# Performance work log

Measured on AMD Instinct MI355X. Metric: run time of the kernel, lower is better.

The kernel has to match this reference:

```python
import jax, jax.numpy as jnp
import numpy as np

COMMITMENT_COST = 0.25


def setup_inputs() -> dict:
    key = jax.random.key(0)
    k1, k2 = jax.random.split(key)
    B, L, D, K = 32, 1024, 128, 1024
    z = jax.random.normal(k1, (B, L, D), dtype=jnp.float32)
    # torch init: uniform_(-1/num_embeddings, 1/num_embeddings)
    codebook = jax.random.uniform(k2, (K, D), dtype=jnp.float32,
                                  minval=-1.0 / K, maxval=1.0 / K)
    return {"z": z, "codebook": codebook}


def reference(z, codebook):
    D = codebook.shape[1]
    flat_z = z.reshape(-1, D)                         # [N, D]
    # squared-euclidean distances, expanded form (same math as torch)
    distances = (jnp.sum(flat_z ** 2, axis=1, keepdims=True)
                 + jnp.sum(codebook ** 2, axis=1)
                 - 2.0 * flat_z @ codebook.T)         # [N, K]
    encoding_indices = jnp.argmin(distances, axis=1)  # [N]
    quantized = codebook[encoding_indices].reshape(z.shape)
    # straight-through estimator
    z_q = z + jax.lax.stop_gradient(quantized - z)
    q_loss = jnp.mean((jax.lax.stop_gradient(quantized) - z) ** 2)
    e_loss = jnp.mean((quantized - jax.lax.stop_gradient(z)) ** 2)
    vq_loss = q_loss + COMMITMENT_COST * e_loss
    return z_q, vq_loss, encoding_indices
```

## Files before the change

kernel.cpp:

```cpp
#include <hip/hip_runtime.h>
#include <float.h>

#define NTOK 32768
#define DDIM 128
#define KCODES 1024
#define TT 128
#define NTHR 512
#define NCHUNK 16
#define CHUNK_BYTES 32768

typedef __attribute__((ext_vector_type(8))) short short8v;
typedef __attribute__((ext_vector_type(4))) float f32x4;

__device__ __forceinline__ float nofuse(float x) { asm volatile("" : "+v"(x)); return x; }

__device__ __forceinline__ unsigned short bf16rne(float x) {
    unsigned int u = __float_as_uint(x);
    unsigned int r = u + 0x7FFFu + ((u >> 16) & 1u);
    return (unsigned short)(r >> 16);
}
__device__ __forceinline__ float bf16tof(unsigned short h) {
    return __uint_as_float(((unsigned int)h) << 16);
}

__device__ __forceinline__ void cvt8(const float* f, uint4& hw, uint4& lw) {
    unsigned int h[8], l[8];
    #pragma unroll
    for (int e = 0; e < 8; ++e) {
        unsigned short hh = bf16rne(f[e]);
        unsigned short ll = bf16rne(f[e] - bf16tof(hh));
        h[e] = hh; l[e] = ll;
    }
    hw = make_uint4(h[0] | (h[1] << 16), h[2] | (h[3] << 16),
                    h[4] | (h[5] << 16), h[6] | (h[7] << 16));
    lw = make_uint4(l[0] | (l[1] << 16), l[2] | (l[3] << 16),
                    l[4] | (l[5] << 16), l[6] | (l[7] << 16));
}

__device__ __forceinline__ short8v as_s8(uint4 v) { return __builtin_bit_cast(short8v, v); }

__global__ __launch_bounds__(256)
void pack_cb(const float* __restrict__ cb, float* __restrict__ cnorm,
             char* __restrict__ cbS) {
    const int tid = threadIdx.x;
    const int row = blockIdx.x * 256 + tid;
    const float* p = cb + (size_t)row * DDIM;
    {
        float r[8];
        {
            float4 a = *(const float4*)p, c = *(const float4*)(p + 4);
            float v[8] = {a.x, a.y, a.z, a.w, c.x, c.y, c.z, c.w};
            #pragma unroll
            for (int j = 0; j < 8; ++j) r[j] = nofuse(v[j] * v[j]);
        }
        #pragma unroll
        for (int i = 8; i < DDIM; i += 8) {
            float4 a = *(const float4*)(p + i), c = *(const float4*)(p + i + 4);
            float v[8] = {a.x, a.y, a.z, a.w, c.x, c.y, c.z, c.w};
            #pragma unroll
            for (int j = 0; j < 8; ++j) r[j] = nofuse(r[j] + nofuse(v[j] * v[j]));
        }
        float s01 = nofuse(r[0] + r[1]), s23 = nofuse(r[2] + r[3]);
        float s45 = nofuse(r[4] + r[5]), s67 = nofuse(r[6] + r[7]);
        cnorm[row] = nofuse(nofuse(s01 + s23) + nofuse(s45 + s67));
    }
    char* base = cbS + (size_t)(row >> 6) * CHUNK_BYTES + (size_t)(row & 63) * 256;
    const int swz = (row & 7) << 4;
    #pragma unroll
    for (int d8 = 0; d8 < 16; ++d8) {
        float4 a = *(const float4*)(p + d8 * 8), c = *(const float4*)(p + d8 * 8 + 4);
        float f[8] = {a.x, a.y, a.z, a.w, c.x, c.y, c.z, c.w};
        uint4 hw, lw;
        cvt8(f, hw, lw);
        int col = (d8 << 4) ^ swz;
        *(uint4*)(base + col) = hw;
        *(uint4*)(base + 16384 + col) = lw;
    }
}

__global__ __launch_bounds__(NTHR, 2)
void dist_argmin(const float* __restrict__ z, const float* __restrict__ cb,
                 const float* __restrict__ cnorm, const char* __restrict__ cbS,
                 float* __restrict__ zq, float* __restrict__ idxf_out,
                 float* __restrict__ partials) {
    __shared__ __align__(16) char buf[2 * CHUNK_BYTES];
    __shared__ float zn_s[TT];
    __shared__ float cn_s[KCODES];
    __shared__ float red_v[TT * 2];
    __shared__ int   red_i[TT * 2];
    __shared__ int   bidx[TT];
    __shared__ float smf[8];

    const int tid  = threadIdx.x;
    const int lane = tid & 63;
    const int wave = tid >> 6;
    const int wy   = wave & 3;
    const int wx   = wave >> 2;
    const int l15  = lane & 15;
    const int l4   = lane >> 4;
    const int t0   = blockIdx.x * TT;

    auto stage = [&](int slot, int chunk) {
        const char* g = cbS + (size_t)chunk * CHUNK_BYTES + wave * 4096 + (lane << 4);
        char* ldst = buf + slot * CHUNK_BYTES + wave * 4096;
        #pragma unroll
        for (int j = 0; j < 4; ++j)
            __builtin_amdgcn_global_load_lds(
                (const __attribute__((address_space(1))) unsigned int*)(g + j * 1024),
                (__attribute__((address_space(3))) unsigned int*)(ldst + j * 1024),
                16, 0, 0);
    };

    short8v Ah[2][4], Al[2][4];
    #pragma unroll
    for (int tf = 0; tf < 2; ++tf) {
        int row = t0 + wy * 32 + tf * 16 + l15;
        const float* p = z + (size_t)row * DDIM;
        #pragma unroll
        for (int ks = 0; ks < 4; ++ks) {
            float4 a = *(const float4*)(p + ks * 32 + l4 * 8);
            float4 c = *(const float4*)(p + ks * 32 + l4 * 8 + 4);
            float f[8] = {a.x, a.y, a.z, a.w, c.x, c.y, c.z, c.w};
            uint4 hw, lw;
            cvt8(f, hw, lw);
            Ah[tf][ks] = as_s8(hw);
            Al[tf][ks] = as_s8(lw);
        }
    }

    stage(0, 0);

    cn_s[tid]       = cnorm[tid];
    cn_s[tid + 512] = cnorm[tid + 512];

    if (tid < TT) {
        const float* p = z + (size_t)(t0 + tid) * DDIM;
        float r[8];
        {
            float4 a = *(const float4*)p, c = *(const float4*)(p + 4);
            float v[8] = {a.x, a.y, a.z, a.w, c.x, c.y, c.z, c.w};
            #pragma unroll
            for (int j = 0; j < 8; ++j) r[j] = nofuse(v[j] * v[j]);
        }
        #pragma unroll
        for (int i = 8; i < DDIM; i += 8) {
            float4 a = *(const float4*)(p + i), c = *(const float4*)(p + i + 4);
            float v[8] = {a.x, a.y, a.z, a.w, c.x, c.y, c.z, c.w};
            #pragma unroll
            for (int j = 0; j < 8; ++j) r[j] = nofuse(r[j] + nofuse(v[j] * v[j]));
        }
        float s01 = nofuse(r[0] + r[1]), s23 = nofuse(r[2] + r[3]);
        float s45 = nofuse(r[4] + r[5]), s67 = nofuse(r[6] + r[7]);
        zn_s[tid] = nofuse(nofuse(s01 + s23) + nofuse(s45 + s67));
    }
    __syncthreads();

    float znr[8];
    #pragma unroll
    for (int tf = 0; tf < 2; ++tf)
        #pragma unroll
        for (int rg = 0; rg < 4; ++rg)
            znr[tf * 4 + rg] = zn_s[wy * 32 + tf * 16 + l4 * 4 + rg];

    float minv[8]; int mini[8];
    #pragma unroll
    for (int i = 0; i < 8; ++i) { minv[i] = FLT_MAX; mini[i] = 0; }

    auto compute = [&](int slot, int it) {
        const char* bb = buf + slot * CHUNK_BYTES;
        short8v Bh[2][4], Bl[2][4];
        #pragma unroll
        for (int cf = 0; cf < 2; ++cf) {
            int r = wx * 32 + cf * 16 + l15;
            int swz = (r & 7) << 4;
            #pragma unroll
            for (int ks = 0; ks < 4; ++ks) {
                int off = r * 256 + ((((ks * 4 + l4) << 4)) ^ swz);
                Bh[cf][ks] = *(const short8v*)(bb + off);
                Bl[cf][ks] = *(const short8v*)(bb + 16384 + off);
            }
        }
        asm volatile("s_waitcnt lgkmcnt(0)" ::: "memory");
        __builtin_amdgcn_sched_barrier(0);

        f32x4 acc[2][2];
        #pragma unroll
        for (int tf = 0; tf < 2; ++tf)
            #pragma unroll
            for (int cf = 0; cf < 2; ++cf)
                acc[tf][cf] = (f32x4){0.f, 0.f, 0.f, 0.f};
        #pragma unroll
        for (int ks = 0; ks < 4; ++ks)
            #pragma unroll
            for (int tf = 0; tf < 2; ++tf)
                #pragma unroll
                for (int cf = 0; cf < 2; ++cf) {
                    acc[tf][cf] = __builtin_amdgcn_mfma_f32_16x16x32_bf16(Ah[tf][ks], Bh[cf][ks], acc[tf][cf], 0, 0, 0);
                    acc[tf][cf] = __builtin_amdgcn_mfma_f32_16x16x32_bf16(Ah[tf][ks], Bl[cf][ks], acc[tf][cf], 0, 0, 0);
                    acc[tf][cf] = __builtin_amdgcn_mfma_f32_16x16x32_bf16(Al[tf][ks], Bh[cf][ks], acc[tf][cf], 0, 0, 0);
                }
        #pragma unroll
        for (int cf = 0; cf < 2; ++cf) {
            int kk = it * 64 + wx * 32 + cf * 16 + l15;
            float cn = cn_s[kk];
            #pragma unroll
            for (int tf = 0; tf < 2; ++tf)
                #pragma unroll
                for (int rg = 0; rg < 4; ++rg) {
                    float s = nofuse(znr[tf * 4 + rg] + cn);
                    float dist = fmaf(-2.0f, acc[tf][cf][rg], s);
                    int ii = tf * 4 + rg;
                    if (dist < minv[ii]) { minv[ii] = dist; mini[ii] = kk; }
                }
        }
    };

    int cur = 0;
    #pragma unroll 1
    for (int t = 0; t < NCHUNK - 1; ++t) {
        stage(cur ^ 1, t + 1);
        asm volatile("s_waitcnt vmcnt(4)" ::: "memory");
        __builtin_amdgcn_s_barrier();
        compute(cur, t);
        asm volatile("s_waitcnt lgkmcnt(0)" ::: "memory");
        __builtin_amdgcn_s_barrier();
        cur ^= 1;
    }
    asm volatile("s_waitcnt vmcnt(0)" ::: "memory");
    __builtin_amdgcn_s_barrier();
    compute(cur, NCHUNK - 1);

    #pragma unroll
    for (int i = 0; i < 8; ++i) {
        float bv = minv[i]; int bi = mini[i];
        #pragma unroll
        for (int off = 1; off < 16; off <<= 1) {
            float ov = __shfl_xor(bv, off);
            int   oi = __shfl_xor(bi, off);
            if (ov < bv || (ov == bv && oi < bi)) { bv = ov; bi = oi; }
        }
        if (l15 == 0) {
            int tok = wy * 32 + (i >> 2) * 16 + l4 * 4 + (i & 3);
            red_v[tok * 2 + wx] = bv;
            red_i[tok * 2 + wx] = bi;
        }
    }
    __syncthreads();
    if (tid < TT) {
        float bv = red_v[tid * 2]; int bi = red_i[tid * 2];
        float v1 = red_v[tid * 2 + 1]; int i1 = red_i[tid * 2 + 1];
        if (v1 < bv || (v1 == bv && i1 < bi)) { bv = v1; bi = i1; }
        bidx[tid] = bi;
        idxf_out[t0 + tid] = (float)bi;
    }
    __syncthreads();

    float s = 0.0f;
    #pragma unroll
    for (int ft = 0; ft < 8; ++ft) {
        int g = ft * NTHR + tid;
        int t = g >> 5;
        int d4 = g & 31;
        int k = bidx[t];
        float4 q4 = *(const float4*)(cb + (size_t)k * DDIM + 4 * d4);
        float4 z4 = *(const float4*)(z + (size_t)(t0 + t) * DDIM + 4 * d4);
        *(float4*)(zq + (size_t)(t0 + t) * DDIM + 4 * d4) = q4;
        float dx = q4.x - z4.x, dy = q4.y - z4.y, dz = q4.z - z4.z, dw = q4.w - z4.w;
        s += dx * dx + dy * dy + dz * dz + dw * dw;
    }
    #pragma unroll
    for (int off = 32; off > 0; off >>= 1) s += __shfl_down(s, off);
    if ((tid & 63) == 0) smf[tid >> 6] = s;
    __syncthreads();
    if (tid == 0) {
        float tot = 0.0f;
        #pragma unroll
        for (int w = 0; w < 8; ++w) tot += smf[w];
        partials[blockIdx.x] = tot;
    }
}

__global__ void loss_final(const float* __restrict__ partials, float* __restrict__ out_loss) {
    double s = 0.0;
    for (int i = threadIdx.x; i < NTOK / TT; i += 256) s += (double)partials[i];
    #pragma unroll
    for (int off = 32; off > 0; off >>= 1) s += __shfl_down(s, off);
    __shared__ double sm[4];
    int lane = threadIdx.x & 63, wv = threadIdx.x >> 6;
    if (lane == 0) sm[wv] = s;
    __syncthreads();
    if (threadIdx.x == 0) {
        double tot = sm[0] + sm[1] + sm[2] + sm[3];
        out_loss[0] = (float)(tot * 1.25 / (double)((size_t)NTOK * DDIM));
    }
}

extern "C" void kernel_launch(void* const* d_in, const int* in_sizes, int n_in,
                              void* d_out, int out_size, void* d_ws, size_t ws_size,
                              hipStream_t stream) {
    const float* z  = (const float*)d_in[0];
    const float* cb = (const float*)d_in[1];
    float* out = (float*)d_out;
    float* zq   = out;
    float* loss = out + (size_t)NTOK * DDIM;
    float* idxf = loss + 1;

    float* cnorm    = (float*)d_ws;
    float* partials = cnorm + KCODES;
    char*  cbS      = (char*)(partials + 256);

    pack_cb<<<KCODES / 256, 256, 0, stream>>>(cb, cnorm, cbS);
    dist_argmin<<<NTOK / TT, NTHR, 0, stream>>>(z, cb, cnorm, cbS, zq, idxf, partials);
    loss_final<<<1, 256, 0, stream>>>(partials, loss);
}
```

Baseline: 123.8 us.

## Remap waves to 2x4 grid with 64 tokens per wave, shrink pack_cb blocks

The wave tiling of the distance GEMM changes from a 4x2 grid (32 tokens x 32 codes per wave) to a 2x4 grid (64 tokens x 16 codes per wave). The z fragments are held in more registers and each B fragment is loaded per k-step and reused across four token tiles, which cuts LDS reads of the codebook per wave. The cross-wave argmin reduction widens to four partials per token, and token norms are read from LDS inside the epilogue instead of being cached in registers. Separately, pack_cb is launched with 64-thread blocks to spread its 1024 rows over more CUs. The larger A register footprint risks spills or lower occupancy under the (512,2) launch bounds.

```diff
diff --git a/kernel.cpp b/kernel.cpp
--- a/kernel.cpp
+++ b/kernel.cpp
@@ -39,11 +39,10 @@
 
 __device__ __forceinline__ short8v as_s8(uint4 v) { return __builtin_bit_cast(short8v, v); }
 
-__global__ __launch_bounds__(256)
+__global__ __launch_bounds__(64)
 void pack_cb(const float* __restrict__ cb, float* __restrict__ cnorm,
              char* __restrict__ cbS) {
-    const int tid = threadIdx.x;
-    const int row = blockIdx.x * 256 + tid;
+    const int row = blockIdx.x * 64 + threadIdx.x;
     const float* p = cb + (size_t)row * DDIM;
     {
         float r[8];
@@ -86,16 +85,16 @@
     __shared__ __align__(16) char buf[2 * CHUNK_BYTES];
     __shared__ float zn_s[TT];
     __shared__ float cn_s[KCODES];
-    __shared__ float red_v[TT * 2];
-    __shared__ int   red_i[TT * 2];
+    __shared__ float red_v[TT * 4];
+    __shared__ int   red_i[TT * 4];
     __shared__ int   bidx[TT];
     __shared__ float smf[8];
 
     const int tid  = threadIdx.x;
     const int lane = tid & 63;
     const int wave = tid >> 6;
-    const int wy   = wave & 3;
-    const int wx   = wave >> 2;
+    const int wy   = wave >> 2;
+    const int wx   = wave & 3;
     const int l15  = lane & 15;
     const int l4   = lane >> 4;
     const int t0   = blockIdx.x * TT;
@@ -111,10 +110,10 @@
                 16, 0, 0);
     };
 
-    short8v Ah[2][4], Al[2][4];
-    #pragma unroll
-    for (int tf = 0; tf < 2; ++tf) {
-        int row = t0 + wy * 32 + tf * 16 + l15;
+    short8v Ah[4][4], Al[4][4];
+    #pragma unroll
+    for (int tf = 0; tf < 4; ++tf) {
+        int row = t0 + wy * 64 + tf * 16 + l15;
         const float* p = z + (size_t)row * DDIM;
         #pragma unroll
         for (int ks = 0; ks < 4; ++ks) {
@@ -155,64 +154,45 @@
     }
     __syncthreads();
 
-    float znr[8];
-    #pragma unroll
-    for (int tf = 0; tf < 2; ++tf)
-        #pragma unroll
-        for (int rg = 0; rg < 4; ++rg)
-            znr[tf * 4 + rg] = zn_s[wy * 32 + tf * 16 + l4 * 4 + rg];
-
-    float minv[8]; int mini[8];
-    #pragma unroll
-    for (int i = 0; i < 8; ++i) { minv[i] = FLT_MAX; mini[i] = 0; }
+    float minv[16]; int mini[16];
+    #pragma unroll
+    for (int i = 0; i < 16; ++i) { minv[i] = FLT_MAX; mini[i] = 0; }
 
     auto compute = [&](int slot, int it) {
         const char* bb = buf + slot * CHUNK_BYTES;
-        short8v Bh[2][4], Bl[2][4];
-        #pragma unroll
-        for (int cf = 0; cf < 2; ++cf) {
-            int r = wx * 32 + cf * 16 + l15;
-            int swz = (r & 7) << 4;
-            #pragma unroll
-            for (int ks = 0; ks < 4; ++ks) {
-                int off = r * 256 + ((((ks * 4 + l4) << 4)) ^ swz);
-                Bh[cf][ks] = *(const short8v*)(bb + off);
-                Bl[cf][ks] = *(const short8v*)(bb + 16384 + off);
+        const int r = wx * 16 + l15;
+        const int swz = (r & 7) << 4;
+        const char* rowp = bb + r * 256;
+
+        f32x4 acc[4];
+        #pragma unroll
+        for (int tf = 0; tf < 4; ++tf) acc[tf] = (f32x4){0.f, 0.f, 0.f, 0.f};
+
+        #pragma unroll
+        for (int ks = 0; ks < 4; ++ks) {
+            int off = (((ks * 4 + l4) << 4)) ^ swz;
+            short8v Bh = *(const short8v*)(rowp + off);
+            short8v Bl = *(const short8v*)(rowp + 16384 + off);
+            #pragma unroll
+            for (int tf = 0; tf < 4; ++tf) {
+                acc[tf] = __builtin_amdgcn_mfma_f32_16x16x32_bf16(Ah[tf][ks], Bh, acc[tf], 0, 0, 0);
+                acc[tf] = __builtin_amdgcn_mfma_f32_16x16x32_bf16(Ah[tf][ks], Bl, acc[tf], 0, 0, 0);
+                acc[tf] = __builtin_amdgcn_mfma_f32_16x16x32_bf16(Al[tf][ks], Bh, acc[tf], 0, 0, 0);
             }
         }
-        asm volatile("s_waitcnt lgkmcnt(0)" ::: "memory");
-        __builtin_amdgcn_sched_barrier(0);
-
-        f32x4 acc[2][2];
-        #pragma unroll
-        for (int tf = 0; tf < 2; ++tf)
-            #pragma unroll
-            for (int cf = 0; cf < 2; ++cf)
-                acc[tf][cf] = (f32x4){0.f, 0.f, 0.f, 0.f};
-        #pragma unroll
-        for (int ks = 0; ks < 4; ++ks)
-            #pragma unroll
-            for (int tf = 0; tf < 2; ++tf)
-                #pragma unroll
-                for (int cf = 0; cf < 2; ++cf) {
-                    acc[tf][cf] = __builtin_amdgcn_mfma_f32_16x16x32_bf16(Ah[tf][ks], Bh[cf][ks], acc[tf][cf], 0, 0, 0);
-                    acc[tf][cf] = __builtin_amdgcn_mfma_f32_16x16x32_bf16(Ah[tf][ks], Bl[cf][ks], acc[tf][cf], 0, 0, 0);
-                    acc[tf][cf] = __builtin_amdgcn_mfma_f32_16x16x32_bf16(Al[tf][ks], Bh[cf][ks], acc[tf][cf], 0, 0, 0);
-                }
-        #pragma unroll
-        for (int cf = 0; cf < 2; ++cf) {
-            int kk = it * 64 + wx * 32 + cf * 16 + l15;
-            float cn = cn_s[kk];
-            #pragma unroll
-            for (int tf = 0; tf < 2; ++tf)
-                #pragma unroll
-                for (int rg = 0; rg < 4; ++rg) {
-                    float s = nofuse(znr[tf * 4 + rg] + cn);
-                    float dist = fmaf(-2.0f, acc[tf][cf][rg], s);
-                    int ii = tf * 4 + rg;
-                    if (dist < minv[ii]) { minv[ii] = dist; mini[ii] = kk; }
-                }
-        }
+
+        int kk = it * 64 + wx * 16 + l15;
+        float cn = cn_s[kk];
+        #pragma unroll
+        for (int tf = 0; tf < 4; ++tf)
+            #pragma unroll
+            for (int rg = 0; rg < 4; ++rg) {
+                float zn = zn_s[wy * 64 + tf * 16 + l4 * 4 + rg];
+                float s = nofuse(zn + cn);
+                float dist = fmaf(-2.0f, acc[tf][rg], s);
+                int ii = tf * 4 + rg;
+                if (dist < minv[ii]) { minv[ii] = dist; mini[ii] = kk; }
+            }
     };
 
     int cur = 0;
@@ -231,7 +211,7 @@
     compute(cur, NCHUNK - 1);
 
     #pragma unroll
-    for (int i = 0; i < 8; ++i) {
+    for (int i = 0; i < 16; ++i) {
         float bv = minv[i]; int bi = mini[i];
         #pragma unroll
         for (int off = 1; off < 16; off <<= 1) {
@@ -240,16 +220,19 @@
             if (ov < bv || (ov == bv && oi < bi)) { bv = ov; bi = oi; }
         }
         if (l15 == 0) {
-            int tok = wy * 32 + (i >> 2) * 16 + l4 * 4 + (i & 3);
-            red_v[tok * 2 + wx] = bv;
-            red_i[tok * 2 + wx] = bi;
+            int tok = wy * 64 + (i >> 2) * 16 + l4 * 4 + (i & 3);
+            red_v[tok * 4 + wx] = bv;
+            red_i[tok * 4 + wx] = bi;
         }
     }
     __syncthreads();
     if (tid < TT) {
-        float bv = red_v[tid * 2]; int bi = red_i[tid * 2];
-        float v1 = red_v[tid * 2 + 1]; int i1 = red_i[tid * 2 + 1];
-        if (v1 < bv || (v1 == bv && i1 < bi)) { bv = v1; bi = i1; }
+        float bv = red_v[tid * 4]; int bi = red_i[tid * 4];
+        #pragma unroll
+        for (int j = 1; j < 4; ++j) {
+            float v = red_v[tid * 4 + j]; int ii = red_i[tid * 4 + j];
+            if (v < bv || (v == bv && ii < bi)) { bv = v; bi = ii; }
+        }
         bidx[tid] = bi;
         idxf_out[t0 + tid] = (float)bi;
     }
@@ -309,7 +292,7 @@
     float* partials = cnorm + KCODES;
     char*  cbS      = (char*)(partials + 256);
 
-    pack_cb<<<KCODES / 256, 256, 0, stream>>>(cb, cnorm, cbS);
+    pack_cb<<<KCODES / 64, 64, 0, stream>>>(cb, cnorm, cbS);
     dist_argmin<<<NTOK / TT, NTHR, 0, stream>>>(z, cb, cnorm, cbS, zq, idxf, partials);
     loss_final<<<1, 256, 0, stream>>>(partials, loss);
 }
```

Result: no change. 122.4 us (-1.1%).
